# Optimization experiments

Measured on AMD Instinct MI355X. Metric: run time of the kernel, lower is better.

## Reference

```python
import jax, jax.numpy as jnp
import numpy as np

N_TOK = 4096   # total packed tokens
HID   = 2048   # n_hidden
NH    = 16     # n_head
HD    = HID // NH  # head_dim = 128
SEQ   = 1024   # per-sequence length (equal-length packing)
NSEQ  = N_TOK // SEQ
EPS   = 1e-6


def setup_inputs() -> dict:
    key = jax.random.key(0)
    ks = jax.random.split(key, 5)
    x = jax.random.normal(ks[0], (N_TOK, HID), jnp.float32)
    Wqkv = jax.random.normal(ks[1], (3 * HID, HID), jnp.float32) * (HID ** -0.5)
    Wo = jax.random.normal(ks[2], (HID, HID), jnp.float32) * (HID ** -0.5)
    gate_w = jax.random.normal(ks[3], (NH, HID), jnp.float32) * 0.02
    gate_b = jnp.zeros((NH,), jnp.float32)
    norm_w = jnp.ones((HD,), jnp.float32)  # RMSNorm weight over head_dim
    # rotary caches: [rope_cache_len, head_dim//2]
    pos = jnp.arange(SEQ, dtype=jnp.float32)
    inv_freq = 1.0 / (10000.0 ** (jnp.arange(0, HD, 2, dtype=jnp.float32) / HD))
    ang = pos[:, None] * inv_freq[None, :]
    cos_cache = jnp.cos(ang)
    sin_cache = jnp.sin(ang)
    cu_seqlens = (jnp.arange(NSEQ + 1, dtype=jnp.int32) * SEQ)
    position_ids = jnp.tile(jnp.arange(SEQ, dtype=jnp.int64), NSEQ)
    return {
        "x": x, "Wqkv": Wqkv, "Wo": Wo, "gate_w": gate_w, "gate_b": gate_b,
        "norm_w": norm_w, "cos_cache": cos_cache, "sin_cache": sin_cache,
        "cu_seqlens": cu_seqlens, "max_seqlen": SEQ, "position_ids": position_ids,
    }


def reference(x, Wqkv, Wo, gate_w, gate_b, norm_w, cos_cache, sin_cache,
              cu_seqlens, max_seqlen, position_ids):
    # fused QKV projection -> [N, 3, H, D]
    qkv = (x @ Wqkv.T).reshape(N_TOK, 3, NH, HD)
    cos = cos_cache[position_ids][:, None, :]  # [N, 1, D//2]
    sin = sin_cache[position_ids][:, None, :]

    def rope(t):  # t: [N, H, D]
        d = HD // 2
        x1, x2 = t[..., :d], t[..., d:]
        return jnp.concatenate([x1 * cos + x2 * sin, -x1 * sin + x2 * cos], axis=-1)

    def rmsnorm(t):  # per-head RMSNorm over D
        return t * jax.lax.rsqrt(jnp.mean(t * t, axis=-1, keepdims=True) + EPS) * norm_w

    q = rmsnorm(rope(qkv[:, 0]))
    k = rmsnorm(rope(qkv[:, 1]))
    v = qkv[:, 2]

    # equal-length packed sequences -> reshape to [B, S, H, D]
    B, S = NSEQ, max_seqlen
    q = q.reshape(B, S, NH, HD)
    k = k.reshape(B, S, NH, HD)
    v = v.reshape(B, S, NH, HD)

    scores = jnp.einsum("bqhd,bkhd->bhqk", q, k) * (HD ** -0.5)
    causal = jnp.tril(jnp.ones((S, S), bool))
    scores = jnp.where(causal, scores, jnp.float32(-1e30))
    probs = jax.nn.softmax(scores, axis=-1)
    attn_out = jnp.einsum("bhqk,bkhd->bqhd", probs, v).reshape(N_TOK, NH, HD)

    gate = jax.nn.sigmoid(x @ gate_w.T + gate_b)[:, :, None]  # [N, H, 1]
    out = (attn_out * gate).reshape(N_TOK, HID)
    return out @ Wo.T
```

## Files before the change

kernel.cpp:

```cpp
#include <hip/hip_runtime.h>
#include <hip/hip_bf16.h>
#include <math.h>

#define N_TOK 4096
#define HID   2048
#define NH    16
#define HD    128
#define SEQ   1024
#define NSEQ  4
#define QKVN  (3*HID)
#define KSPLIT (3*HID)

typedef __bf16 bf16x8 __attribute__((ext_vector_type(8)));
typedef float  f32x4  __attribute__((ext_vector_type(4)));
typedef unsigned short ushort8v __attribute__((ext_vector_type(8)));

#define MFMA16(a,b,c) __builtin_amdgcn_mfma_f32_16x16x32_bf16(a,b,c,0,0,0)

__device__ __forceinline__ ushort bf16_rn(float f) {
  unsigned u = __float_as_uint(f);
  return (ushort)((u + 0x7FFFu + ((u >> 16) & 1u)) >> 16);
}
__device__ __forceinline__ float bf16_tof(ushort h) {
  return __uint_as_float(((unsigned)h) << 16);
}
__device__ __forceinline__ void gload16(const void* g, void* l) {
  __builtin_amdgcn_global_load_lds(
      (const __attribute__((address_space(1))) void*)g,
      (__attribute__((address_space(3))) void*)l, 16, 0, 0);
}

__global__ __launch_bounds__(256)
void split_bf16(const float* __restrict__ src, ushort* __restrict__ dst,
                int total4, int amode) {
  for (int idx = blockIdx.x * 256 + threadIdx.x; idx < total4;
       idx += gridDim.x * 256) {
    const int r = idx >> 9, kq = idx & 511;
    float4 v = ((const float4*)src)[idx];
    float f[4] = {v.x, v.y, v.z, v.w};
    ushort h[4], lo[4];
    #pragma unroll
    for (int j = 0; j < 4; ++j) {
      h[j]  = bf16_rn(f[j]);
      lo[j] = bf16_rn(f[j] - bf16_tof(h[j]));
    }
    ushort4 hv = make_ushort4(h[0], h[1], h[2], h[3]);
    ushort4 lv = make_ushort4(lo[0], lo[1], lo[2], lo[3]);
    ushort* row = dst + (size_t)r * KSPLIT + kq * 4;
    *(ushort4*)(row)        = hv;
    *(ushort4*)(row + 2048) = amode ? hv : lv;
    *(ushort4*)(row + 4096) = amode ? lv : hv;
  }
}

__global__ __launch_bounds__(256)
void gemm_bf16_nt(const ushort* __restrict__ A, const ushort* __restrict__ B,
                  float* __restrict__ C, int M, int N, int K) {
  __shared__ ushort As[128 * 32];
  __shared__ ushort Bs[128 * 32];
  const int nx = gridDim.x;
  const int nwg = nx * gridDim.y;
  const int bid = blockIdx.y * nx + blockIdx.x;
  const int cpx = nwg >> 3;
  const int swz = (bid & 7) * cpx + (bid >> 3);
  const int bx = swz % nx, by = swz / nx;
  const int tid = threadIdx.x;
  const int w = tid >> 6, l = tid & 63;
  const int wm = w >> 1, wn = w & 1;
  const int m0 = by * 128, n0 = bx * 128;
  const int lr = l & 15;
  const int ko = (l >> 4) * 8;
  const int srow = l >> 2;
  const int scol = (l & 3) * 8;

  f32x4 acc[4][4];
  #pragma unroll
  for (int m = 0; m < 4; ++m)
    #pragma unroll
    for (int n = 0; n < 4; ++n)
      acc[m][n] = (f32x4){0.f, 0.f, 0.f, 0.f};

  for (int k0 = 0; k0 < K; k0 += 32) {
    #pragma unroll
    for (int i = 0; i < 2; ++i) {
      const int rbase = w * 32 + i * 16;
      const ushort* ga = A + (size_t)(m0 + rbase + srow) * K + k0 + scol;
      const ushort* gb = B + (size_t)(n0 + rbase + srow) * K + k0 + scol;
      gload16(ga, &As[rbase * 32]);
      gload16(gb, &Bs[rbase * 32]);
    }
    __syncthreads();
    bf16x8 av[4], bv[4];
    #pragma unroll
    for (int m = 0; m < 4; ++m)
      av[m] = *(const bf16x8*)&As[(wm * 64 + m * 16 + lr) * 32 + ko];
    #pragma unroll
    for (int n = 0; n < 4; ++n)
      bv[n] = *(const bf16x8*)&Bs[(wn * 64 + n * 16 + lr) * 32 + ko];
    #pragma unroll
    for (int m = 0; m < 4; ++m)
      #pragma unroll
      for (int n = 0; n < 4; ++n)
        acc[m][n] = MFMA16(av[m], bv[n], acc[m][n]);
    __syncthreads();
  }
  const int crow = (l >> 4) * 4, ccol = l & 15;
  #pragma unroll
  for (int m = 0; m < 4; ++m)
    #pragma unroll
    for (int n = 0; n < 4; ++n) {
      #pragma unroll
      for (int j = 0; j < 4; ++j)
        C[(size_t)(m0 + wm * 64 + m * 16 + crow + j) * N +
          (n0 + wn * 64 + n * 16 + ccol)] = acc[m][n][j];
    }
}

__global__ __launch_bounds__(256)
void rope_split(const float* __restrict__ qkv, const float* __restrict__ norm_w,
                const float* __restrict__ cosc, const float* __restrict__ sinc,
                const int* __restrict__ cu,
                ushort* __restrict__ Qsp, ushort* __restrict__ Ksp) {
  const int wid  = blockIdx.x * 4 + (threadIdx.x >> 6);
  const int lane = threadIdx.x & 63;
  const int t   = wid >> 5;
  const int rem = wid & 31;
  const int s   = rem >> 4;
  const int h   = rem & 15;
  const int pos = t - cu[t >> 10];
  const float* p = qkv + (size_t)t * QKVN + s * HID + h * HD;
  float x1 = p[lane], x2 = p[lane + 64];
  float c  = cosc[pos * 64 + lane];
  float sn = sinc[pos * 64 + lane];
  float y1 = x1 * c + x2 * sn;
  float y2 = x2 * c - x1 * sn;
  float ss = y1 * y1 + y2 * y2;
  #pragma unroll
  for (int o = 32; o > 0; o >>= 1) ss += __shfl_xor(ss, o, 64);
  float r = rsqrtf(ss * (1.0f / 128.0f) + 1e-6f);
  const float sc = s ? 1.0f : 0.08838834764831845f;
  float o1 = y1 * r * norm_w[lane] * sc;
  float o2 = y2 * r * norm_w[lane + 64] * sc;
  ushort h1 = bf16_rn(o1), l1 = bf16_rn(o1 - bf16_tof(h1));
  ushort h2 = bf16_rn(o2), l2 = bf16_rn(o2 - bf16_tof(h2));
  char* db = (char*)((s ? Ksp : Qsp) + ((size_t)t * NH + h) * 256);
  const int b0 = (lane * 2) ^ ((t & 7) << 4);
  *(ushort*)(db + b0)       = h1;
  *(ushort*)(db + 128 + b0) = h2;
  *(ushort*)(db + 256 + b0) = l1;
  *(ushort*)(db + 384 + b0) = l2;
}

__global__ __launch_bounds__(256)
void v_split_t(const float* __restrict__ qkv, ushort* __restrict__ Vt) {
  __shared__ float Vb[64][133];
  const int kt = blockIdx.x, bh = blockIdx.y;
  const int b = bh >> 4, h = bh & 15;
  const int tid = threadIdx.x;
  {
    const int k = tid >> 5, dm = (tid & 31) * 4;
    const float* src = qkv + (size_t)(b * SEQ + kt * 64) * QKVN + 2 * HID + h * HD;
    #pragma unroll
    for (int i = 0; i < 8; ++i) {
      float4 v = *(const float4*)(src + (size_t)(i * 8 + k) * QKVN + dm);
      Vb[i * 8 + k][dm]     = v.x;
      Vb[i * 8 + k][dm + 1] = v.y;
      Vb[i * 8 + k][dm + 2] = v.z;
      Vb[i * 8 + k][dm + 3] = v.w;
    }
  }
  __syncthreads();
  const int c  = tid & 7;
  const int d0 = tid >> 3;
  char* base = (char*)Vt + (size_t)bh * 256 * 2048;
  #pragma unroll
  for (int it = 0; it < 4; ++it) {
    const int d = d0 + it * 32;
    ushort8v vh, vl;
    #pragma unroll
    for (int j = 0; j < 8; ++j) {
      float f = Vb[c * 8 + j][d];
      ushort hh = bf16_rn(f);
      vh[j] = hh;
      vl[j] = bf16_rn(f - bf16_tof(hh));
    }
    const int cc = (c ^ (d & 7)) * 16;
    *(ushort8v*)(base + (size_t)d * 2048 + kt * 128 + cc)        = vh;
    *(ushort8v*)(base + (size_t)(128 + d) * 2048 + kt * 128 + cc) = vl;
  }
}

__global__ __launch_bounds__(256)
void gate_kernel(const float* __restrict__ x, const float* __restrict__ gw,
                 const float* __restrict__ gb, float* __restrict__ gate) {
  __shared__ float xs[HID];
  const int t = blockIdx.x, tid = threadIdx.x;
  *(float4*)&xs[tid * 8]     = *(const float4*)&x[(size_t)t * HID + tid * 8];
  *(float4*)&xs[tid * 8 + 4] = *(const float4*)&x[(size_t)t * HID + tid * 8 + 4];
  __syncthreads();
  const int h = tid >> 4, i = tid & 15;
  const float* w  = gw + (size_t)h * HID + i * 128;
  const float* xx = xs + i * 128;
  float sum = 0.f;
  #pragma unroll
  for (int j = 0; j < 128; j += 4) {
    float4 wv = *(const float4*)(w + j);
    float4 xv = *(const float4*)(xx + j);
    sum += wv.x * xv.x + wv.y * xv.y + wv.z * xv.z + wv.w * xv.w;
  }
  sum += __shfl_xor(sum, 8, 64);
  sum += __shfl_xor(sum, 4, 64);
  sum += __shfl_xor(sum, 2, 64);
  sum += __shfl_xor(sum, 1, 64);
  if (i == 0) gate[t * NH + h] = 1.f / (1.f + __expf(-(sum + gb[h])));
}

__global__ __launch_bounds__(256, 1)
void attn_mfma(const ushort* __restrict__ Qsp, const ushort* __restrict__ Ksp,
               const ushort* __restrict__ Vtg, const float* __restrict__ gate,
               float* __restrict__ og) {
  __shared__ ushort Qs[64 * 256];
  __shared__ ushort Ks[64 * 256];
  __shared__ ushort Vs[256 * 64];
  __shared__ float  SP[64 * 66];
  __shared__ float  cf[64];
  const int bh = blockIdx.x, b = bh >> 4, h = bh & 15;
  const int qt = (int)gridDim.y - 1 - (int)blockIdx.y;
  const int tid = threadIdx.x;
  const int w = tid >> 6, l = tid & 63;
  const int wm = w >> 1, wn = w & 1;
  const int fr = l & 15;
  const int fk = (l >> 4) * 16;
  const int swr = (fr & 7) << 4;
  const int crow = (l >> 4) * 4, ccol = l & 15;
  const int sr = tid >> 2, so = tid & 3;

  {
    const char* qg = (const char*)Qsp + ((size_t)(b * SEQ + qt * 64) * 16 + h) * 512
                     + (size_t)w * 131072 + (size_t)(l >> 5) * 8192 + (l & 31) * 16;
    char* qd = (char*)Qs + w * 8192;
    #pragma unroll
    for (int i = 0; i < 8; ++i) gload16(qg + i * 16384, qd + i * 1024);
  }
  const char* kg = (const char*)Ksp + ((size_t)(b * SEQ) * 16 + h) * 512
                   + (size_t)w * 131072 + (size_t)(l >> 5) * 8192 + (l & 31) * 16;
  const char* vg = (const char*)Vtg + ((size_t)bh * 256 + w * 64 + (l >> 3)) * 2048
                   + (l & 7) * 16;
  char* kd = (char*)Ks + w * 8192;
  char* vd = (char*)Vs + w * 8192;

  f32x4 acc_o[2][4];
  #pragma unroll
  for (int mi = 0; mi < 2; ++mi)
    #pragma unroll
    for (int ni = 0; ni < 4; ++ni)
      acc_o[mi][ni] = (f32x4){0.f, 0.f, 0.f, 0.f};
  float m_run = -INFINITY, l_run = 0.f;

  for (int kt = 0; kt <= qt; ++kt) {
    #pragma unroll
    for (int i = 0; i < 8; ++i) gload16(kg + i * 16384, kd + i * 1024);
    #pragma unroll
    for (int i = 0; i < 8; ++i) gload16(vg + i * 16384, vd + i * 1024);
    kg += 524288;
    vg += 128;
    __syncthreads();

    f32x4 acc_s[2][2];
    #pragma unroll
    for (int mi = 0; mi < 2; ++mi)
      #pragma unroll
      for (int ni = 0; ni < 2; ++ni)
        acc_s[mi][ni] = (f32x4){0.f, 0.f, 0.f, 0.f};
    #pragma unroll
    for (int term = 0; term < 3; ++term) {
      const int qo = (term == 2) ? 256 : 0;
      const int ko2 = (term == 1) ? 256 : 0;
      #pragma unroll
      for (int ks = 0; ks < 4; ++ks) {
        const int ia = (qo + ks * 64 + fk) ^ swr;
        const int ib = (ko2 + ks * 64 + fk) ^ swr;
        bf16x8 a0 = *(const bf16x8*)((const char*)Qs + (wm * 32 + fr) * 512 + ia);
        bf16x8 a1 = *(const bf16x8*)((const char*)Qs + (wm * 32 + 16 + fr) * 512 + ia);
        bf16x8 b0 = *(const bf16x8*)((const char*)Ks + (wn * 32 + fr) * 512 + ib);
        bf16x8 b1 = *(const bf16x8*)((const char*)Ks + (wn * 32 + 16 + fr) * 512 + ib);
        acc_s[0][0] = MFMA16(a0, b0, acc_s[0][0]);
        acc_s[0][1] = MFMA16(a0, b1, acc_s[0][1]);
        acc_s[1][0] = MFMA16(a1, b0, acc_s[1][0]);
        acc_s[1][1] = MFMA16(a1, b1, acc_s[1][1]);
      }
    }
    #pragma unroll
    for (int mi = 0; mi < 2; ++mi)
      #pragma unroll
      for (int ni = 0; ni < 2; ++ni)
        #pragma unroll
        for (int j = 0; j < 4; ++j)
          SP[(wm * 32 + mi * 16 + crow + j) * 66 + wn * 32 + ni * 16 + ccol] =
              acc_s[mi][ni][j];
    __syncthreads();

    float s[16];
    #pragma unroll
    for (int j = 0; j < 16; ++j) s[j] = SP[sr * 66 + so * 16 + j];
    __syncthreads();

    {
      if (kt == qt) {
        #pragma unroll
        for (int j = 0; j < 16; ++j)
          if (so * 16 + j > sr) s[j] = -INFINITY;
      }
      float mx = -INFINITY;
      #pragma unroll
      for (int j = 0; j < 16; ++j) mx = fmaxf(mx, s[j]);
      mx = fmaxf(mx, __shfl_xor(mx, 1, 64));
      mx = fmaxf(mx, __shfl_xor(mx, 2, 64));
      float mnew = fmaxf(m_run, mx);
      float corr = __expf(m_run - mnew);
      float p[16];
      float ls = 0.f;
      #pragma unroll
      for (int j = 0; j < 16; ++j) { p[j] = __expf(s[j] - mnew); ls += p[j]; }
      ls += __shfl_xor(ls, 1, 64);
      ls += __shfl_xor(ls, 2, 64);
      l_run = l_run * corr + ls;
      m_run = mnew;
      char* prow = (char*)SP + sr * 256;
      const int swp = (sr & 7) << 4;
      #pragma unroll
      for (int half = 0; half < 2; ++half) {
        ushort8v vh, vl;
        #pragma unroll
        for (int j = 0; j < 8; ++j) {
          float pv = p[half * 8 + j];
          ushort hh = bf16_rn(pv);
          vh[j] = hh;
          vl[j] = bf16_rn(pv - bf16_tof(hh));
        }
        const int cb = (so * 32 + half * 16) ^ swp;
        *(ushort8v*)(prow + cb)       = vh;
        *(ushort8v*)(prow + 128 + cb) = vl;
      }
      if (so == 0) cf[sr] = corr;
    }
    __syncthreads();

    {
      float cl[8];
      #pragma unroll
      for (int mi = 0; mi < 2; ++mi)
        #pragma unroll
        for (int j = 0; j < 4; ++j)
          cl[mi * 4 + j] = cf[wm * 32 + mi * 16 + crow + j];
      #pragma unroll
      for (int mi = 0; mi < 2; ++mi)
        #pragma unroll
        for (int ni = 0; ni < 4; ++ni)
          #pragma unroll
          for (int j = 0; j < 4; ++j)
            acc_o[mi][ni][j] *= cl[mi * 4 + j];
      #pragma unroll
      for (int term = 0; term < 3; ++term) {
        const int po = (term == 2) ? 128 : 0;
        const int vo = (term == 1) ? 128 : 0;
        #pragma unroll
        for (int ks = 0; ks < 2; ++ks) {
          const int ip = (ks * 64 + fk) ^ swr;
          bf16x8 pa0 = *(const bf16x8*)((const char*)SP + (wm * 32 + fr) * 256 + po + ip);
          bf16x8 pa1 = *(const bf16x8*)((const char*)SP + (wm * 32 + 16 + fr) * 256 + po + ip);
          #pragma unroll
          for (int ni = 0; ni < 4; ++ni) {
            const int dr = vo + wn * 64 + ni * 16 + fr;
            bf16x8 vv = *(const bf16x8*)((const char*)Vs + dr * 128 + ((ks * 64 + fk) ^ swr));
            acc_o[0][ni] = MFMA16(pa0, vv, acc_o[0][ni]);
            acc_o[1][ni] = MFMA16(pa1, vv, acc_o[1][ni]);
          }
        }
      }
    }
    __syncthreads();
  }

  if (so == 0) {
    const int t = b * SEQ + qt * 64 + sr;
    cf[sr] = gate[t * NH + h] / l_run;
  }
  __syncthreads();
  {
    float rf[8];
    #pragma unroll
    for (int mi = 0; mi < 2; ++mi)
      #pragma unroll
      for (int j = 0; j < 4; ++j)
        rf[mi * 4 + j] = cf[wm * 32 + mi * 16 + crow + j];
    #pragma unroll
    for (int mi = 0; mi < 2; ++mi)
      #pragma unroll
      for (int ni = 0; ni < 4; ++ni)
        #pragma unroll
        for (int j = 0; j < 4; ++j)
          og[(size_t)(b * SEQ + qt * 64 + wm * 32 + mi * 16 + crow + j) * HID
             + h * HD + wn * 64 + ni * 16 + ccol] = acc_o[mi][ni][j] * rf[mi * 4 + j];
  }
}

extern "C" void kernel_launch(void* const* d_in, const int* in_sizes, int n_in,
                              void* d_out, int out_size, void* d_ws, size_t ws_size,
                              hipStream_t stream) {
  const float* x    = (const float*)d_in[0];
  const float* Wqkv = (const float*)d_in[1];
  const float* Wo   = (const float*)d_in[2];
  const float* gw   = (const float*)d_in[3];
  const float* gb   = (const float*)d_in[4];
  const float* nw   = (const float*)d_in[5];
  const float* cosc = (const float*)d_in[6];
  const float* sinc = (const float*)d_in[7];
  const int*   cu   = (const int*)d_in[8];
  float* out = (float*)d_out;

  float*  qkv  = (float*)d_ws;
  float*  attn = qkv + (size_t)N_TOK * QKVN;
  float*  gate = attn + (size_t)N_TOK * HID;
  ushort* Abuf = (ushort*)(gate + (size_t)N_TOK * NH);
  ushort* Bbuf = Abuf + (size_t)N_TOK * KSPLIT;
  ushort* Qsp = Abuf;
  ushort* Ksp = Bbuf;
  ushort* Vt  = Bbuf + (size_t)N_TOK * NH * 256;

  split_bf16<<<2048, 256, 0, stream>>>(x,    Abuf, N_TOK * HID / 4, 1);
  split_bf16<<<2048, 256, 0, stream>>>(Wqkv, Bbuf, QKVN * HID / 4, 0);
  gemm_bf16_nt<<<dim3(QKVN / 128, N_TOK / 128), 256, 0, stream>>>(
      Abuf, Bbuf, qkv, N_TOK, QKVN, KSPLIT);

  rope_split<<<dim3(N_TOK * 2 * NH / 4), 256, 0, stream>>>(qkv, nw, cosc, sinc,
                                                           cu, Qsp, Ksp);
  v_split_t<<<dim3(16, 64), 256, 0, stream>>>(qkv, Vt);
  gate_kernel<<<dim3(N_TOK), 256, 0, stream>>>(x, gw, gb, gate);

  attn_mfma<<<dim3(NSEQ * NH, SEQ / 64), 256, 0, stream>>>(Qsp, Ksp, Vt, gate, attn);

  split_bf16<<<2048, 256, 0, stream>>>(attn, Abuf, N_TOK * HID / 4, 1);
  split_bf16<<<2048, 256, 0, stream>>>(Wo,   Bbuf, HID * HID / 4, 0);
  gemm_bf16_nt<<<dim3(HID / 128, N_TOK / 128), 256, 0, stream>>>(
      Abuf, Bbuf, out, N_TOK, HID, KSPLIT);
}
```

Baseline: 976.4 us.

## Replace QKV GEMM with 256x256-tile double-buffered MFMA kernel

Adds a new bf16 NT GEMM kernel for the QKV projection. It uses 256x256 output tiles, 512 threads and 128KB of dynamic LDS. Tiles are double-buffered through direct global-to-LDS loads with an XOR swizzle, explicit vmcnt waits, scheduling barriers and priority raising around the MFMA blocks. The goal is more data reuse per tile and better overlap of loads with matrix math than the 128x128 kernel gave. The trade-offs are larger-grid tail effects (384 blocks, one block per CU because of the LDS size) and fragile hand-written synchronisation.

After: 875.7 us. 1.11x faster.

```diff
diff --git a/kernel.cpp b/kernel.cpp
--- a/kernel.cpp
+++ b/kernel.cpp
@@ -29,6 +29,13 @@
       (const __attribute__((address_space(1))) void*)g,
       (__attribute__((address_space(3))) void*)l, 16, 0, 0);
 }
+
+#define CFENCE asm volatile("" ::: "memory")
+#define BARR do { __builtin_amdgcn_sched_barrier(0); CFENCE; \
+                  __builtin_amdgcn_s_barrier(); CFENCE; \
+                  __builtin_amdgcn_sched_barrier(0); } while (0)
+#define VMCNT4 do { __builtin_amdgcn_sched_barrier(0); \
+                    asm volatile("s_waitcnt vmcnt(4)" ::: "memory"); } while (0)
 
 __global__ __launch_bounds__(256)
 void split_bf16(const float* __restrict__ src, ushort* __restrict__ dst,
@@ -51,6 +58,120 @@
     *(ushort4*)(row + 2048) = amode ? hv : lv;
     *(ushort4*)(row + 4096) = amode ? lv : hv;
   }
+}
+
+__global__ __launch_bounds__(512, 2)
+void gemm256(const ushort* __restrict__ A, const ushort* __restrict__ B,
+             float* __restrict__ C, int M, int N, int K) {
+  extern __shared__ ushort lds[];
+  const int nx = gridDim.x;
+  const int nwg = nx * gridDim.y;
+  const int bid = blockIdx.y * nx + blockIdx.x;
+  const int cpx = nwg >> 3;
+  const int swz = (bid & 7) * cpx + (bid >> 3);
+  const int bx = swz % nx, by = swz / nx;
+  const int m0 = by * 256, n0 = bx * 256;
+  const int tid = threadIdx.x;
+  const int w = tid >> 6, l = tid & 63;
+  const int wm = w >> 2, wn = w & 3;
+  const int fr = l & 15, kc = l >> 4;
+  const int cx = (kc ^ ((fr >> 1) & 3)) * 8;
+  const int aoff = (wm * 128 + fr) * 32 + cx;
+  const int boff = 16384 + (wn * 64 + fr) * 32 + cx;
+  const int tr0 = tid >> 2;
+  const int q0c = tid & 3;
+  const int wub = (tid & 448) * 8;
+  const int NTILE = K >> 6;
+
+  auto stage = [&](int bufus, int kt, int s) {
+    const int koe = kt * 64 + s * 32;
+    #pragma unroll
+    for (int i = 0; i < 2; ++i) {
+      const int tr = i * 128 + tr0;
+      const int gq = (q0c ^ ((tr >> 1) & 3)) * 8;
+      gload16(A + (size_t)(m0 + tr) * K + koe + gq,
+              &lds[bufus + s * 8192 + i * 8192 / 2 * 0 + (i * 512) * 8 + wub]);
+    }
+    #pragma unroll
+    for (int i = 0; i < 2; ++i) {
+      const int tr = i * 128 + tr0;
+      const int gq = (q0c ^ ((tr >> 1) & 3)) * 8;
+      gload16(B + (size_t)(n0 + tr) * K + koe + gq,
+              &lds[bufus + 16384 + s * 8192 + (i * 512) * 8 + wub]);
+    }
+  };
+  auto lda4 = [&](bf16x8* dst, int cb, int s, int mbase) {
+    #pragma unroll
+    for (int m = 0; m < 4; ++m)
+      dst[m] = *(const bf16x8*)&lds[cb + s * 8192 + aoff + (mbase + m) * 512];
+  };
+  auto ldb4 = [&](bf16x8* dst, int cb, int s) {
+    #pragma unroll
+    for (int n = 0; n < 4; ++n)
+      dst[n] = *(const bf16x8*)&lds[cb + s * 8192 + boff + n * 512];
+  };
+
+  f32x4 acc[8][4];
+  #pragma unroll
+  for (int m = 0; m < 8; ++m)
+    #pragma unroll
+    for (int n = 0; n < 4; ++n)
+      acc[m][n] = (f32x4){0.f, 0.f, 0.f, 0.f};
+
+  auto mm = [&](bf16x8* av_, bf16x8* bv_, int mbase) {
+    __builtin_amdgcn_s_setprio(1);
+    #pragma unroll
+    for (int m = 0; m < 4; ++m)
+      #pragma unroll
+      for (int n = 0; n < 4; ++n)
+        acc[mbase + m][n] = MFMA16(av_[m], bv_[n], acc[mbase + m][n]);
+    __builtin_amdgcn_s_setprio(0);
+  };
+
+  stage(0, 0, 0);
+  stage(0, 0, 1);
+  VMCNT4;
+  BARR;
+
+  for (int T = 0; T < NTILE; ++T) {
+    const int cb = (T & 1) << 15;
+    const int nb = 32768 - cb;
+    const bool st = (T + 1) < NTILE;
+    bf16x8 a0[4], b0[4], a1[4];
+    lda4(a0, cb, 0, 0);
+    ldb4(b0, cb, 0);
+    if (st) stage(nb, T + 1, 0);
+    BARR;
+    mm(a0, b0, 0);
+    BARR;
+    lda4(a1, cb, 0, 4);
+    VMCNT4;
+    BARR;
+    mm(a1, b0, 4);
+    BARR;
+    lda4(a0, cb, 1, 0);
+    ldb4(b0, cb, 1);
+    if (st) stage(nb, T + 1, 1);
+    BARR;
+    mm(a0, b0, 0);
+    BARR;
+    lda4(a1, cb, 1, 4);
+    VMCNT4;
+    BARR;
+    mm(a1, b0, 4);
+    BARR;
+  }
+
+  const int crow = (l >> 4) * 4, ccol = l & 15;
+  #pragma unroll
+  for (int m = 0; m < 8; ++m)
+    #pragma unroll
+    for (int n = 0; n < 4; ++n) {
+      #pragma unroll
+      for (int j = 0; j < 4; ++j)
+        C[(size_t)(m0 + wm * 128 + m * 16 + crow + j) * N +
+          (n0 + wn * 64 + n * 16 + ccol)] = acc[m][n][j];
+    }
 }
 
 __global__ __launch_bounds__(256)
@@ -428,9 +549,12 @@
   ushort* Ksp = Bbuf;
   ushort* Vt  = Bbuf + (size_t)N_TOK * NH * 256;
 
+  (void)hipFuncSetAttribute((const void*)gemm256,
+                            hipFuncAttributeMaxDynamicSharedMemorySize, 131072);
+
   split_bf16<<<2048, 256, 0, stream>>>(x,    Abuf, N_TOK * HID / 4, 1);
   split_bf16<<<2048, 256, 0, stream>>>(Wqkv, Bbuf, QKVN * HID / 4, 0);
-  gemm_bf16_nt<<<dim3(QKVN / 128, N_TOK / 128), 256, 0, stream>>>(
+  gemm256<<<dim3(QKVN / 256, N_TOK / 256), 512, 131072, stream>>>(
       Abuf, Bbuf, qkv, N_TOK, QKVN, KSPLIT);
 
   rope_split<<<dim3(N_TOK * 2 * NH / 4), 256, 0, stream>>>(qkv, nw, cosc, sinc,
```
